# Optimization experiments

Measured on AMD Instinct MI355X. Metric: run time of the kernel, lower is better.

The kernel has to match this reference:

```python
import jax, jax.numpy as jnp
import numpy as np

B, S, D, H = 8, 512, 1024, 16
HD = D // H                      # head_dim = 64
MAX_SEQ_LEN = 512
SCRATCH_SLOTS = 64


def _rope_cache():
    inv_freq = 1.0 / (10000.0 ** (jnp.arange(0, HD, 2, dtype=jnp.float32) / HD))
    t = jnp.arange(MAX_SEQ_LEN + SCRATCH_SLOTS, dtype=jnp.float32)
    freqs = jnp.outer(t, inv_freq)               # [T, HD//2]
    freqs = jnp.concatenate([freqs, freqs], -1)  # [T, HD]
    return jnp.sin(freqs), jnp.cos(freqs)


def rotate_half(x):
    x1, x2 = x[..., : x.shape[-1] // 2], x[..., x.shape[-1] // 2 :]
    return jnp.concatenate([-x2, x1], axis=-1)


def setup_inputs() -> dict:
    key = jax.random.key(0)
    ks = jax.random.split(key, 5)
    def w(k):
        return jax.random.normal(k, (D, D), dtype=jnp.float32) * 0.02
    return {
        "x": jax.random.normal(ks[0], (B, S, D), dtype=jnp.float32),
        "Wq": w(ks[1]), "bq": jnp.zeros((D,), jnp.float32),
        "Wk": w(ks[2]), "bk": jnp.zeros((D,), jnp.float32),
        "Wv": w(ks[3]), "bv": jnp.zeros((D,), jnp.float32),
        "Wo": w(ks[4]), "bo": jnp.zeros((D,), jnp.float32),
    }


def reference(x, Wq, bq, Wk, bk, Wv, bv, Wo, bo):
    b, s, d = x.shape
    sin_c, cos_c = _rope_cache()
    scale = jnp.array(HD ** (-0.5), dtype=jnp.float32)

    xh = x.astype(jnp.float16)
    def lin(inp, W, bias):  # nnx.Linear with dtype=fp16: cast params + input to fp16
        return inp @ W.astype(jnp.float16) + bias.astype(jnp.float16)

    q = lin(xh, Wq, bq).reshape(b, s, H, HD)
    k = lin(xh, Wk, bk).reshape(b, s, H, HD)
    v = lin(xh, Wv, bv).reshape(b, s, H, HD)

    sin = sin_c[:s, None, :].astype(jnp.float32)  # [s,1,HD]
    cos = cos_c[:s, None, :].astype(jnp.float32)
    qf = q.astype(jnp.float32)
    kf = k.astype(jnp.float32)
    q = qf * cos + rotate_half(qf) * sin
    k = kf * cos + rotate_half(kf) * sin
    v = v.astype(jnp.float32)
    q = q * scale  # module's explicit scale

    # [b,H,s,HD]
    q, k, v = (t.transpose(0, 2, 1, 3) for t in (q, k, v))

    # jax.nn.dot_product_attention additionally scales by 1/sqrt(HD)
    logits = jnp.einsum("bhqd,bhkd->bhqk", q, k) * scale
    probs = jax.nn.softmax(logits, axis=-1)
    out = jnp.einsum("bhqk,bhkd->bhqd", probs, v)
    out = out.transpose(0, 2, 1, 3).reshape(b, s, d)
    return lin(out.astype(jnp.float16), Wo, bo)
```

## Files before the change

kernel.cpp:

```cpp
#include <hip/hip_runtime.h>

typedef _Float16 half8 __attribute__((ext_vector_type(8)));
typedef _Float16 half4v __attribute__((ext_vector_type(4)));
typedef float f32x4 __attribute__((ext_vector_type(4)));

#define OFF_CS    0u
#define OFF_XH    (1u<<20)
#define OFF_WQKVT (OFF_XH + 8u*1024u*1024u)
#define OFF_WOT   (OFF_WQKVT + 8u*1024u*1024u)
#define OFF_QKV   (OFF_WOT + 2u*1024u*1024u)
#define OFF_VT    OFF_XH
#define OFF_ATTN  OFF_WQKVT

__device__ __forceinline__ void gload16(const _Float16* g, _Float16* l) {
  __builtin_amdgcn_global_load_lds((const __attribute__((address_space(1))) void*)g,
                                   (__attribute__((address_space(3))) void*)l, 16, 0, 0);
}

__global__ void prep_k(const float* __restrict__ x,
                       const float* __restrict__ W0, const float* __restrict__ W1,
                       const float* __restrict__ W2, const float* __restrict__ W3,
                       _Float16* __restrict__ xh, _Float16* __restrict__ wqkvt,
                       _Float16* __restrict__ wot, float2* __restrict__ cs) {
  int bid = blockIdx.x, tid = threadIdx.x;
  if (bid < 4096) {
    int i = bid * 256 + tid;
    float4 v = ((const float4*)x)[i];
    half4v h;
    h[0] = (_Float16)v.x; h[1] = (_Float16)v.y; h[2] = (_Float16)v.z; h[3] = (_Float16)v.w;
    *(half4v*)(xh + (size_t)i * 4) = h;
  } else if (bid < 8192) {
    __shared__ float tile[32][33];
    int tb = bid - 4096;
    int z = tb >> 10, t = tb & 1023, by = t >> 5, bx = t & 31;
    const float* W = z == 0 ? W0 : z == 1 ? W1 : z == 2 ? W2 : W3;
    _Float16* Wt = z < 3 ? wqkvt + (size_t)z * 1048576 : wot;
    int r = tid >> 3, c0 = (tid & 7) * 4;
    float4 v = *(const float4*)(W + (size_t)(by * 32 + r) * 1024 + bx * 32 + c0);
    tile[r][c0] = v.x; tile[r][c0 + 1] = v.y; tile[r][c0 + 2] = v.z; tile[r][c0 + 3] = v.w;
    __syncthreads();
    half4v h;
#pragma unroll
    for (int j = 0; j < 4; j++) h[j] = (_Float16)tile[c0 + j][r];
    *(half4v*)(Wt + (size_t)(bx * 32 + r) * 1024 + by * 32 + c0) = h;
  } else {
    int idx = (bid - 8192) * 256 + tid;
    int pos = idx >> 5, j = idx & 31;
    float inv = powf(10000.0f, -(float)j * (1.0f / 32.0f));
    float f = (float)pos * inv;
    cs[idx] = make_float2(cosf(f), sinf(f));
  }
}

template <int MODE>
__global__ __launch_bounds__(256, 3) void gemm128_k(
    const _Float16* __restrict__ A, const _Float16* __restrict__ Bt,
    const float* __restrict__ b0, const float* __restrict__ b1, const float* __restrict__ b2,
    void* __restrict__ Cv, const float2* __restrict__ cs) {
  const int K = 1024;
  const int N = (MODE == 0) ? 3072 : 1024;
  const int NBX = N / 128;
  __shared__ _Float16 Ab[2][128 * 32];
  __shared__ _Float16 Bb[2][128 * 32];

  int nwg = gridDim.x, cpx = nwg >> 3;
  int bid = blockIdx.x;
  int wgid = (bid & 7) * cpx + (bid >> 3);
  int by = wgid / NBX, bx = wgid % NBX;

  int tid = threadIdx.x, lane = tid & 63, w = tid >> 6;
  int wr = w >> 1, wc = w & 1;
  int arow = lane & 15, ag = lane >> 4;
  int s8 = (((arow & 1) << 2) | ag) ^ ((arow >> 1) & 7);

  int qq = (lane & 7) ^ (lane >> 3);
  int rloc = ((lane >> 3) << 1) + (qq >> 2);
  int gcol = (qq & 3) * 8;

  const _Float16* Ag = A + (size_t)(by * 128) * K;
  const _Float16* Bg = Bt + (size_t)(bx * 128) * K;

  f32x4 acc[4][4] = {};

  {
    int k0 = 0;
#pragma unroll
    for (int i = 0; i < 2; i++) {
      int c = w * 2 + i;
      gload16(Ag + (size_t)(c * 16 + rloc) * K + k0 + gcol, &Ab[0][c * 512]);
      gload16(Bg + (size_t)(c * 16 + rloc) * K + k0 + gcol, &Bb[0][c * 512]);
    }
  }
  __syncthreads();

  for (int t = 0; t < 32; ++t) {
    int cur = t & 1;
    if (t < 31) {
      int k0 = (t + 1) * 32;
#pragma unroll
      for (int i = 0; i < 2; i++) {
        int c = w * 2 + i;
        gload16(Ag + (size_t)(c * 16 + rloc) * K + k0 + gcol, &Ab[cur ^ 1][c * 512]);
        gload16(Bg + (size_t)(c * 16 + rloc) * K + k0 + gcol, &Bb[cur ^ 1][c * 512]);
      }
    }
    __builtin_amdgcn_sched_barrier(0);
    const _Float16* Ac = &Ab[cur][0];
    const _Float16* Bc = &Bb[cur][0];
    half8 a[4], b[4];
#pragma unroll
    for (int m = 0; m < 4; m++) {
      int R = wr * 64 + m * 16 + arow;
      a[m] = *(const half8*)&Ac[(R >> 1) * 64 + s8 * 8];
    }
#pragma unroll
    for (int n = 0; n < 4; n++) {
      int R = wc * 64 + n * 16 + arow;
      b[n] = *(const half8*)&Bc[(R >> 1) * 64 + s8 * 8];
    }
#pragma unroll
    for (int m = 0; m < 4; m++)
#pragma unroll
      for (int n = 0; n < 4; n++)
        acc[m][n] = __builtin_amdgcn_mfma_f32_16x16x32_f16(a[m], b[n], acc[m][n], 0, 0, 0);
    __syncthreads();
  }

  int gc0 = bx * 128 + wc * 64;
  if (MODE == 0) {
    const float* bp = gc0 < 1024 ? b0 : (gc0 < 2048 ? b1 : b2);
    float bb_[4];
#pragma unroll
    for (int n = 0; n < 4; n++) bb_[n] = bp[(gc0 & 1023) + n * 16 + arow];
    _Float16* C = (_Float16*)Cv;
    if (gc0 < 2048) {
      bool isQ = gc0 < 1024;
#pragma unroll
      for (int m = 0; m < 4; m++) {
        int gr = by * 128 + wr * 64 + m * 16 + ag * 4;
#pragma unroll
        for (int r = 0; r < 4; r++) {
          int row = gr + r, pos = row & 511;
#pragma unroll
          for (int n = 0; n < 2; n++) {
            int j = n * 16 + arow;
            float av = (float)(_Float16)(acc[m][n][r] + bb_[n]);
            float bv = (float)(_Float16)(acc[m][n + 2][r] + bb_[n + 2]);
            float2 tt = cs[pos * 32 + j];
            float o0 = av * tt.x - bv * tt.y;
            float o1 = bv * tt.x + av * tt.y;
            if (isQ) { o0 *= 0.015625f; o1 *= 0.015625f; }
            C[(size_t)row * 3072 + gc0 + j]      = (_Float16)o0;
            C[(size_t)row * 3072 + gc0 + j + 32] = (_Float16)o1;
          }
        }
      }
    } else {
#pragma unroll
      for (int m = 0; m < 4; m++) {
        int gr = by * 128 + wr * 64 + m * 16 + ag * 4;
#pragma unroll
        for (int n = 0; n < 4; n++)
#pragma unroll
          for (int r = 0; r < 4; r++)
            C[(size_t)(gr + r) * 3072 + gc0 + n * 16 + arow] = (_Float16)(acc[m][n][r] + bb_[n]);
      }
    }
  } else {
    float* C = (float*)Cv;
#pragma unroll
    for (int m = 0; m < 4; m++) {
      int gr = by * 128 + wr * 64 + m * 16 + ag * 4;
#pragma unroll
      for (int n = 0; n < 4; n++) {
        int gc = gc0 + n * 16 + arow;
        float bb = b0[gc];
#pragma unroll
        for (int r = 0; r < 4; r++)
          C[(size_t)(gr + r) * 1024 + gc] = (float)(_Float16)(acc[m][n][r] + bb);
      }
    }
  }
}

__global__ void vt_k(const _Float16* __restrict__ qkv, _Float16* __restrict__ VT) {
  __shared__ _Float16 T[64][72];
  int id = blockIdx.x;
  int bh = id & 127, sb = id >> 7;
  int b = bh >> 4, h = bh & 15;
  int tid = threadIdx.x;
  const _Float16* src = qkv + (size_t)(b * 512 + sb * 64) * 3072 + 2048 + h * 64;
#pragma unroll
  for (int i = 0; i < 2; i++) {
    int c = i * 256 + tid, r = c >> 3, cc = c & 7;
    *(half8*)&T[r][cc * 8] = *(const half8*)(src + (size_t)r * 3072 + cc * 8);
  }
  __syncthreads();
  _Float16* dst = VT + (size_t)bh * 64 * 512 + (size_t)sb * 64;
#pragma unroll
  for (int i = 0; i < 2; i++) {
    int c = i * 256 + tid, hd = c >> 3, sc = c & 7;
    half8 v;
#pragma unroll
    for (int j = 0; j < 8; j++) v[j] = T[sc * 8 + j][hd];
    *(half8*)(dst + (size_t)hd * 512 + sc * 8) = v;
  }
}

__global__ __launch_bounds__(256, 4) void attn_k(const _Float16* __restrict__ qkv,
                                                 const _Float16* __restrict__ VT,
                                                 _Float16* __restrict__ out) {
  int id = blockIdx.x;
  int bh = id & 127, qt = id >> 7;
  int b = bh >> 4, h = bh & 15;
  int tid = threadIdx.x, lane = tid & 63, w = tid >> 6;
  int arow = lane & 15, ag = lane >> 4;

  __shared__ _Float16 Ks[64 * 64];
  __shared__ _Float16 Vs[64 * 64];
  __shared__ _Float16 Pl[4][16][72];

  int qrow0 = b * 512 + qt * 64 + w * 16;
  const _Float16* Qp = qkv + (size_t)qrow0 * 3072 + h * 64;
  half8 qa[2];
#pragma unroll
  for (int ks = 0; ks < 2; ks++)
    qa[ks] = *(const half8*)(Qp + (size_t)arow * 3072 + ks * 32 + ag * 8);

  const _Float16* Kb = qkv + (size_t)(b * 512) * 3072 + 1024 + h * 64;
  const _Float16* Vb = VT + (size_t)bh * 64 * 512;

  int srow = lane >> 3;
  int sslot = (lane & 7) ^ srow;
  const _Float16* Ksrc0 = Kb + (size_t)(w * 16 + srow) * 3072 + sslot * 8;
  const _Float16* Vsrc0 = Vb + (size_t)(w * 16 + srow) * 512 + sslot * 8;

  int rs = arow & 7;

  float psl[4] = {0.f, 0.f, 0.f, 0.f};
  f32x4 oacc[4] = {};

  for (int st = 0; st < 8; ++st) {
#pragma unroll
    for (int i = 0; i < 2; i++) {
      gload16(Ksrc0 + (size_t)(st * 64 + i * 8) * 3072, &Ks[(w * 16 + i * 8) * 64]);
      gload16(Vsrc0 + (size_t)(i * 8) * 512 + st * 64,  &Vs[(w * 16 + i * 8) * 64]);
    }
    __syncthreads();

    f32x4 lg[4];
#pragma unroll
    for (int c = 0; c < 4; c++) {
      f32x4 a0 = {};
#pragma unroll
      for (int ks = 0; ks < 2; ks++) {
        int slot = (ks * 4 + ag) ^ rs;
        half8 kb = *(const half8*)&Ks[(c * 16 + arow) * 64 + slot * 8];
        a0 = __builtin_amdgcn_mfma_f32_16x16x32_f16(qa[ks], kb, a0, 0, 0, 0);
      }
      lg[c] = a0;
    }
    _Float16 ph[4][4];
#pragma unroll
    for (int r = 0; r < 4; r++) {
#pragma unroll
      for (int c = 0; c < 4; c++) {
        float p = __builtin_amdgcn_exp2f(lg[c][r] * 1.44269504f);
        psl[r] += p;
        ph[c][r] = (_Float16)p;
      }
    }
#pragma unroll
    for (int c = 0; c < 4; c++)
#pragma unroll
      for (int r = 0; r < 4; r++) Pl[w][ag * 4 + r][c * 16 + arow] = ph[c][r];
#pragma unroll
    for (int ks = 0; ks < 2; ks++) {
      half8 pa = *(const half8*)&Pl[w][arow][ks * 32 + ag * 8];
#pragma unroll
      for (int c = 0; c < 4; c++) {
        int slot = (ks * 4 + ag) ^ rs;
        half8 vb = *(const half8*)&Vs[(c * 16 + arow) * 64 + slot * 8];
        oacc[c] = __builtin_amdgcn_mfma_f32_16x16x32_f16(pa, vb, oacc[c], 0, 0, 0);
      }
    }
    __syncthreads();
  }
#pragma unroll
  for (int r = 0; r < 4; r++)
#pragma unroll
    for (int d = 1; d < 16; d <<= 1) psl[r] += __shfl_xor(psl[r], d, 16);
#pragma unroll
  for (int c = 0; c < 4; c++)
#pragma unroll
    for (int r = 0; r < 4; r++) {
      float v = oacc[c][r] / psl[r];
      out[(size_t)(qrow0 + ag * 4 + r) * 1024 + h * 64 + c * 16 + arow] = (_Float16)v;
    }
}

extern "C" void kernel_launch(void* const* d_in, const int* in_sizes, int n_in,
                              void* d_out, int out_size, void* d_ws, size_t ws_size,
                              hipStream_t stream) {
  const float* x  = (const float*)d_in[0];
  const float* Wq = (const float*)d_in[1];
  const float* bq = (const float*)d_in[2];
  const float* Wk = (const float*)d_in[3];
  const float* bk = (const float*)d_in[4];
  const float* Wv = (const float*)d_in[5];
  const float* bv = (const float*)d_in[6];
  const float* Wo = (const float*)d_in[7];
  const float* bo = (const float*)d_in[8];

  char* ws = (char*)d_ws;
  float2* cs      = (float2*)(ws + OFF_CS);
  _Float16* xh    = (_Float16*)(ws + OFF_XH);
  _Float16* wqkvt = (_Float16*)(ws + OFF_WQKVT);
  _Float16* wot   = (_Float16*)(ws + OFF_WOT);
  _Float16* qkv   = (_Float16*)(ws + OFF_QKV);
  _Float16* VT    = (_Float16*)(ws + OFF_VT);
  _Float16* attn  = (_Float16*)(ws + OFF_ATTN);

  prep_k<<<8256, 256, 0, stream>>>(x, Wq, Wk, Wv, Wo, xh, wqkvt, wot, cs);
  gemm128_k<0><<<768, 256, 0, stream>>>(xh, wqkvt, bq, bk, bv, qkv, cs);
  vt_k<<<1024, 256, 0, stream>>>(qkv, VT);
  attn_k<<<1024, 256, 0, stream>>>(qkv, VT, attn);
  gemm128_k<1><<<256, 256, 0, stream>>>(attn, wot, bo, bo, bo, d_out, cs);
}
```

Before: 96.88 us.

## Triple-buffer GEMM loads, split K/V waits in attention, halve out-proj tile

The GEMM moves from a double to a triple-buffered LDS ring with two stages in flight. It replaces __syncthreads with explicit vmcnt waits plus raw barriers and raises wave priority around the MFMA blocks. The output projection uses 64-row tiles, doubling its grid to 512 blocks so more CUs are busy. Attention double-buffers K and waits on V separately, so the logits MFMAs overlap the V load. This adds LDS use and relies on hand-counted vmcnt values, which could be wrong if the compiler emits extra loads.

```diff
diff --git a/kernel.cpp b/kernel.cpp
--- a/kernel.cpp
+++ b/kernel.cpp
@@ -53,15 +53,17 @@
 }
 
 template <int MODE>
-__global__ __launch_bounds__(256, 3) void gemm128_k(
+__global__ __launch_bounds__(256, MODE == 0 ? 3 : 2) void gemm_k(
     const _Float16* __restrict__ A, const _Float16* __restrict__ Bt,
     const float* __restrict__ b0, const float* __restrict__ b1, const float* __restrict__ b2,
     void* __restrict__ Cv, const float2* __restrict__ cs) {
-  const int K = 1024;
-  const int N = (MODE == 0) ? 3072 : 1024;
-  const int NBX = N / 128;
-  __shared__ _Float16 Ab[2][128 * 32];
-  __shared__ _Float16 Bb[2][128 * 32];
+  constexpr int BM  = (MODE == 0) ? 128 : 64;
+  constexpr int N   = (MODE == 0) ? 3072 : 1024;
+  constexpr int NBX = N / 128;
+  constexpr int MF  = BM / 32;
+  constexpr int ACH = BM / 64;
+  __shared__ _Float16 Ar[3][BM * 32];
+  __shared__ _Float16 Br[3][128 * 32];
 
   int nwg = gridDim.x, cpx = nwg >> 3;
   int bid = blockIdx.x;
@@ -77,40 +79,41 @@
   int rloc = ((lane >> 3) << 1) + (qq >> 2);
   int gcol = (qq & 3) * 8;
 
-  const _Float16* Ag = A + (size_t)(by * 128) * K;
-  const _Float16* Bg = Bt + (size_t)(bx * 128) * K;
-
-  f32x4 acc[4][4] = {};
-
-  {
-    int k0 = 0;
+  const _Float16* Ag = A + (size_t)(by * BM) * 1024;
+  const _Float16* Bg = Bt + (size_t)(bx * 128) * 1024;
+
+  f32x4 acc[MF][4] = {};
+
+  auto stage = [&](int t) {
+    int slot = t % 3;
+    int k0 = t * 32;
+#pragma unroll
+    for (int i = 0; i < ACH; i++) {
+      int c = w * ACH + i;
+      gload16(Ag + (size_t)(c * 16 + rloc) * 1024 + k0 + gcol, &Ar[slot][c * 512]);
+    }
 #pragma unroll
     for (int i = 0; i < 2; i++) {
       int c = w * 2 + i;
-      gload16(Ag + (size_t)(c * 16 + rloc) * K + k0 + gcol, &Ab[0][c * 512]);
-      gload16(Bg + (size_t)(c * 16 + rloc) * K + k0 + gcol, &Bb[0][c * 512]);
-    }
-  }
-  __syncthreads();
+      gload16(Bg + (size_t)(c * 16 + rloc) * 1024 + k0 + gcol, &Br[slot][c * 512]);
+    }
+  };
+
+  stage(0); stage(1);
+  if (MODE == 0) asm volatile("s_waitcnt vmcnt(4)" ::: "memory");
+  else           asm volatile("s_waitcnt vmcnt(3)" ::: "memory");
+  __builtin_amdgcn_s_barrier();
+  __builtin_amdgcn_sched_barrier(0);
 
   for (int t = 0; t < 32; ++t) {
-    int cur = t & 1;
-    if (t < 31) {
-      int k0 = (t + 1) * 32;
-#pragma unroll
-      for (int i = 0; i < 2; i++) {
-        int c = w * 2 + i;
-        gload16(Ag + (size_t)(c * 16 + rloc) * K + k0 + gcol, &Ab[cur ^ 1][c * 512]);
-        gload16(Bg + (size_t)(c * 16 + rloc) * K + k0 + gcol, &Bb[cur ^ 1][c * 512]);
-      }
-    }
-    __builtin_amdgcn_sched_barrier(0);
-    const _Float16* Ac = &Ab[cur][0];
-    const _Float16* Bc = &Bb[cur][0];
-    half8 a[4], b[4];
-#pragma unroll
-    for (int m = 0; m < 4; m++) {
-      int R = wr * 64 + m * 16 + arow;
+    if (t < 30) stage(t + 2);
+    __builtin_amdgcn_sched_barrier(0);
+    const _Float16* Ac = &Ar[t % 3][0];
+    const _Float16* Bc = &Br[t % 3][0];
+    half8 a[MF], b[4];
+#pragma unroll
+    for (int m = 0; m < MF; m++) {
+      int R = wr * (BM / 2) + m * 16 + arow;
       a[m] = *(const half8*)&Ac[(R >> 1) * 64 + s8 * 8];
     }
 #pragma unroll
@@ -118,12 +121,24 @@
       int R = wc * 64 + n * 16 + arow;
       b[n] = *(const half8*)&Bc[(R >> 1) * 64 + s8 * 8];
     }
-#pragma unroll
-    for (int m = 0; m < 4; m++)
+    __builtin_amdgcn_s_setprio(1);
+#pragma unroll
+    for (int m = 0; m < MF; m++)
 #pragma unroll
       for (int n = 0; n < 4; n++)
         acc[m][n] = __builtin_amdgcn_mfma_f32_16x16x32_f16(a[m], b[n], acc[m][n], 0, 0, 0);
-    __syncthreads();
+    __builtin_amdgcn_s_setprio(0);
+    __builtin_amdgcn_sched_barrier(0);
+    if (t < 30) {
+      if (MODE == 0) asm volatile("s_waitcnt vmcnt(4)" ::: "memory");
+      else           asm volatile("s_waitcnt vmcnt(3)" ::: "memory");
+    } else if (t == 30) {
+      asm volatile("s_waitcnt vmcnt(0)" ::: "memory");
+    }
+    if (t < 31) {
+      __builtin_amdgcn_s_barrier();
+      __builtin_amdgcn_sched_barrier(0);
+    }
   }
 
   int gc0 = bx * 128 + wc * 64;
@@ -136,8 +151,8 @@
     if (gc0 < 2048) {
       bool isQ = gc0 < 1024;
 #pragma unroll
-      for (int m = 0; m < 4; m++) {
-        int gr = by * 128 + wr * 64 + m * 16 + ag * 4;
+      for (int m = 0; m < MF; m++) {
+        int gr = by * BM + wr * (BM / 2) + m * 16 + ag * 4;
 #pragma unroll
         for (int r = 0; r < 4; r++) {
           int row = gr + r, pos = row & 511;
@@ -157,8 +172,8 @@
       }
     } else {
 #pragma unroll
-      for (int m = 0; m < 4; m++) {
-        int gr = by * 128 + wr * 64 + m * 16 + ag * 4;
+      for (int m = 0; m < MF; m++) {
+        int gr = by * BM + wr * (BM / 2) + m * 16 + ag * 4;
 #pragma unroll
         for (int n = 0; n < 4; n++)
 #pragma unroll
@@ -169,8 +184,8 @@
   } else {
     float* C = (float*)Cv;
 #pragma unroll
-    for (int m = 0; m < 4; m++) {
-      int gr = by * 128 + wr * 64 + m * 16 + ag * 4;
+    for (int m = 0; m < MF; m++) {
+      int gr = by * BM + wr * (BM / 2) + m * 16 + ag * 4;
 #pragma unroll
       for (int n = 0; n < 4; n++) {
         int gc = gc0 + n * 16 + arow;
@@ -216,7 +231,7 @@
   int tid = threadIdx.x, lane = tid & 63, w = tid >> 6;
   int arow = lane & 15, ag = lane >> 4;
 
-  __shared__ _Float16 Ks[64 * 64];
+  __shared__ _Float16 Kb2[2][64 * 64];
   __shared__ _Float16 Vs[64 * 64];
   __shared__ _Float16 Pl[4][16][72];
 
@@ -227,37 +242,50 @@
   for (int ks = 0; ks < 2; ks++)
     qa[ks] = *(const half8*)(Qp + (size_t)arow * 3072 + ks * 32 + ag * 8);
 
-  const _Float16* Kb = qkv + (size_t)(b * 512) * 3072 + 1024 + h * 64;
-  const _Float16* Vb = VT + (size_t)bh * 64 * 512;
+  const _Float16* Kg = qkv + (size_t)(b * 512) * 3072 + 1024 + h * 64;
+  const _Float16* Vg = VT + (size_t)bh * 64 * 512;
 
   int srow = lane >> 3;
   int sslot = (lane & 7) ^ srow;
-  const _Float16* Ksrc0 = Kb + (size_t)(w * 16 + srow) * 3072 + sslot * 8;
-  const _Float16* Vsrc0 = Vb + (size_t)(w * 16 + srow) * 512 + sslot * 8;
+  const _Float16* Ksrc0 = Kg + (size_t)(w * 16 + srow) * 3072 + sslot * 8;
+  const _Float16* Vsrc0 = Vg + (size_t)(w * 16 + srow) * 512 + sslot * 8;
 
   int rs = arow & 7;
 
   float psl[4] = {0.f, 0.f, 0.f, 0.f};
   f32x4 oacc[4] = {};
 
+#pragma unroll
+  for (int i = 0; i < 2; i++)
+    gload16(Ksrc0 + (size_t)(i * 8) * 3072, &Kb2[0][(w * 16 + i * 8) * 64]);
+  asm volatile("s_waitcnt vmcnt(0)" ::: "memory");
+  __builtin_amdgcn_s_barrier();
+  __builtin_amdgcn_sched_barrier(0);
+
   for (int st = 0; st < 8; ++st) {
 #pragma unroll
-    for (int i = 0; i < 2; i++) {
-      gload16(Ksrc0 + (size_t)(st * 64 + i * 8) * 3072, &Ks[(w * 16 + i * 8) * 64]);
-      gload16(Vsrc0 + (size_t)(i * 8) * 512 + st * 64,  &Vs[(w * 16 + i * 8) * 64]);
-    }
-    __syncthreads();
-
+    for (int i = 0; i < 2; i++)
+      gload16(Vsrc0 + (size_t)(i * 8) * 512 + st * 64, &Vs[(w * 16 + i * 8) * 64]);
+    if (st < 7) {
+#pragma unroll
+      for (int i = 0; i < 2; i++)
+        gload16(Ksrc0 + (size_t)((st + 1) * 64 + i * 8) * 3072,
+                &Kb2[(st + 1) & 1][(w * 16 + i * 8) * 64]);
+    }
+    __builtin_amdgcn_sched_barrier(0);
+    const _Float16* Kc = &Kb2[st & 1][0];
     f32x4 lg[4];
 #pragma unroll
     for (int c = 0; c < 4; c++) {
       f32x4 a0 = {};
+      __builtin_amdgcn_s_setprio(1);
 #pragma unroll
       for (int ks = 0; ks < 2; ks++) {
         int slot = (ks * 4 + ag) ^ rs;
-        half8 kb = *(const half8*)&Ks[(c * 16 + arow) * 64 + slot * 8];
+        half8 kb = *(const half8*)&Kc[(c * 16 + arow) * 64 + slot * 8];
         a0 = __builtin_amdgcn_mfma_f32_16x16x32_f16(qa[ks], kb, a0, 0, 0, 0);
       }
+      __builtin_amdgcn_s_setprio(0);
       lg[c] = a0;
     }
     _Float16 ph[4][4];
@@ -274,17 +302,29 @@
     for (int c = 0; c < 4; c++)
 #pragma unroll
       for (int r = 0; r < 4; r++) Pl[w][ag * 4 + r][c * 16 + arow] = ph[c][r];
+    __builtin_amdgcn_sched_barrier(0);
+    if (st < 7) asm volatile("s_waitcnt vmcnt(2)" ::: "memory");
+    else        asm volatile("s_waitcnt vmcnt(0)" ::: "memory");
+    __builtin_amdgcn_s_barrier();
+    __builtin_amdgcn_sched_barrier(0);
 #pragma unroll
     for (int ks = 0; ks < 2; ks++) {
       half8 pa = *(const half8*)&Pl[w][arow][ks * 32 + ag * 8];
+      __builtin_amdgcn_s_setprio(1);
 #pragma unroll
       for (int c = 0; c < 4; c++) {
         int slot = (ks * 4 + ag) ^ rs;
         half8 vb = *(const half8*)&Vs[(c * 16 + arow) * 64 + slot * 8];
         oacc[c] = __builtin_amdgcn_mfma_f32_16x16x32_f16(pa, vb, oacc[c], 0, 0, 0);
       }
-    }
-    __syncthreads();
+      __builtin_amdgcn_s_setprio(0);
+    }
+    __builtin_amdgcn_sched_barrier(0);
+    if (st < 7) {
+      asm volatile("s_waitcnt vmcnt(0)" ::: "memory");
+      __builtin_amdgcn_s_barrier();
+      __builtin_amdgcn_sched_barrier(0);
+    }
   }
 #pragma unroll
   for (int r = 0; r < 4; r++)
@@ -322,8 +362,8 @@
   _Float16* attn  = (_Float16*)(ws + OFF_ATTN);
 
   prep_k<<<8256, 256, 0, stream>>>(x, Wq, Wk, Wv, Wo, xh, wqkvt, wot, cs);
-  gemm128_k<0><<<768, 256, 0, stream>>>(xh, wqkvt, bq, bk, bv, qkv, cs);
+  gemm_k<0><<<768, 256, 0, stream>>>(xh, wqkvt, bq, bk, bv, qkv, cs);
   vt_k<<<1024, 256, 0, stream>>>(qkv, VT);
   attn_k<<<1024, 256, 0, stream>>>(qkv, VT, attn);
-  gemm128_k<1><<<256, 256, 0, stream>>>(attn, wot, bo, bo, bo, d_out, cs);
-}
+  gemm_k<1><<<512, 256, 0, stream>>>(attn, wot, bo, bo, bo, d_out, cs);
+}
```

Result: slower. 106.4 us (+9.8%).
